# Kernel optimization log

Hardware: AMD Instinct MI355X
Metric: run time of the kernel (lower is better)

## Reference

```python
import jax, jax.numpy as jnp
import numpy as np

B, T, D, H, DFF = 64, 100, 1024, 16, 4096
HD = D // H
EPS = 1e-5


def _rope_tables(t_len, hd, dtype):
    # matches RotaryEmbedding: inv_freq over even dims, emb = cat([freqs, freqs])
    inv_freq = 1.0 / (10000.0 ** (jnp.arange(0, hd, 2, dtype=jnp.float32) / hd))
    t = jnp.arange(t_len, dtype=jnp.float32)
    freqs = jnp.einsum('i,j->ij', t, inv_freq)          # (T, hd/2)
    emb = jnp.concatenate([freqs, freqs], axis=-1)      # (T, hd)
    # apply_rope uses cos[..., ::2] / sin[..., ::2]
    cos = jnp.cos(emb)[:, ::2].astype(dtype)            # (T, hd/2)
    sin = jnp.sin(emb)[:, ::2].astype(dtype)
    return cos, sin


def _apply_rope(x, cos, sin):
    # x: (B, H, T, hd); cos/sin: (T, hd/2) broadcast over B,H
    x1 = x[..., ::2]
    x2 = x[..., 1::2]
    return jnp.concatenate([x1 * cos - x2 * sin, x1 * sin + x2 * cos], axis=-1)


def _layernorm(x, g, b):
    mu = jnp.mean(x, axis=-1, keepdims=True)
    var = jnp.mean(jnp.square(x - mu), axis=-1, keepdims=True)
    return (x - mu) * jax.lax.rsqrt(var + EPS) * g + b


def setup_inputs() -> dict:
    key = jax.random.key(0)
    ks = jax.random.split(key, 8)
    s = 0.02
    return {
        'tgt': jax.random.normal(ks[0], (B, T, D), dtype=jnp.float32),
        'Wqkv': jax.random.normal(ks[1], (3 * D, D), dtype=jnp.float32) * s,
        'bqkv': jnp.zeros((3 * D,), jnp.float32),
        'Wo': jax.random.normal(ks[2], (D, D), dtype=jnp.float32) * s,
        'bo': jnp.zeros((D,), jnp.float32),
        'W1': jax.random.normal(ks[3], (DFF, D), dtype=jnp.float32) * s,
        'b1': jnp.zeros((DFF,), jnp.float32),
        'W2': jax.random.normal(ks[4], (D, DFF), dtype=jnp.float32) * s,
        'b2': jnp.zeros((D,), jnp.float32),
        'g1': jnp.ones((D,), jnp.float32),
        'be1': jnp.zeros((D,), jnp.float32),
        'g2': jnp.ones((D,), jnp.float32),
        'be2': jnp.zeros((D,), jnp.float32),
        'tgt_mask': jnp.tril(jnp.ones((T, T), jnp.int32)),
    }


def reference(tgt, Wqkv, bqkv, Wo, bo, W1, b1, W2, b2, g1, be1, g2, be2, tgt_mask):
    dtype = tgt.dtype
    # QKV projection (torch Linear: x @ W.T + b)
    qkv = jnp.einsum('btd,ed->bte', tgt, Wqkv) + bqkv          # (B,T,3D)
    qkv = qkv.reshape(B, T, 3, H, HD).transpose(2, 0, 3, 1, 4)  # (3,B,H,T,hd)
    q, k, v = qkv[0], qkv[1], qkv[2]

    cos, sin = _rope_tables(T, HD, dtype)
    q = _apply_rope(q, cos, sin)
    k = _apply_rope(k, cos, sin)

    scale = 1.0 / np.sqrt(HD)
    scores = jnp.einsum('bhqd,bhkd->bhqk', q, k) * scale        # (B,H,T,T)
    scores = jnp.where(tgt_mask == 0, -jnp.inf, scores)
    attn = jax.nn.softmax(scores, axis=-1)
    ctx = jnp.einsum('bhqk,bhkd->bhqd', attn, v)                # (B,H,T,hd)
    ctx = ctx.transpose(0, 2, 1, 3).reshape(B, T, D)

    tgt2 = jnp.einsum('btd,ed->bte', ctx, Wo) + bo
    x = _layernorm(tgt + tgt2, g1, be1)

    h = jax.nn.relu(jnp.einsum('btd,fd->btf', x, W1) + b1)
    ff = jnp.einsum('btf,df->btd', h, W2) + b2
    out = _layernorm(x + ff, g2, be2)
    return out
```

## Files before the change

kernel.cpp:

```cpp
#include <hip/hip_runtime.h>
#include <math.h>

#define Bn   64
#define Tn   100
#define Tp   128
#define Dn   1024
#define Hn   16
#define HDn  64
#define DFFn 4096
#define EPSf 1e-5f

typedef unsigned short ushort_t;
typedef __attribute__((ext_vector_type(8))) __bf16 bf16x8;
typedef __attribute__((ext_vector_type(4))) float f32x4;

__device__ __forceinline__ float u2f(ushort_t u) {
    union { unsigned int i; float f; } v; v.i = ((unsigned int)u) << 16; return v.f;
}
__device__ __forceinline__ ushort_t f2bf(float f) {
    union { float f; unsigned int u; } v; v.f = f;
    unsigned int r = v.u + 0x7FFFu + ((v.u >> 16) & 1u);
    return (ushort_t)(r >> 16);
}

__device__ __forceinline__ void gload_lds16(const void* g, void* l) {
    __builtin_amdgcn_global_load_lds(
        (const __attribute__((address_space(1))) unsigned int*)g,
        (__attribute__((address_space(3))) unsigned int*)l,
        16, 0, 0);
}

#define VMWAIT_(n) asm volatile("s_waitcnt vmcnt(" #n ")" ::: "memory")
#define VMWAIT(n)  VMWAIT_(n)

struct ConvSeg { const float* src; ushort_t* dst; int n4; };
struct Conv5   { ConvSeg seg[5]; };

__global__ __launch_bounds__(256) void conv_bf16_multi(Conv5 cfg)
{
    int i = blockIdx.x * 256 + threadIdx.x;
    #pragma unroll
    for (int s = 0; s < 5; ++s) {
        const int n = cfg.seg[s].n4;
        if (i < n) {
            float4 v = ((const float4*)cfg.seg[s].src)[i];
            ushort4 o;
            o.x = f2bf(v.x); o.y = f2bf(v.y); o.z = f2bf(v.z); o.w = f2bf(v.w);
            ((ushort4*)cfg.seg[s].dst)[i] = o;
            return;
        }
        i -= n;
    }
}

#define GEMM_TILE_MAP(gx_, gy_, swz_)                                        \
    const int L  = blockIdx.x;                                               \
    int rowt, colt;                                                          \
    if (swz_) {                                                              \
        const int group = L / (8 * (gx_));                                   \
        int l = L - group * 8 * (gx_);                                       \
        const int rem = (gy_) - group * 8;                                   \
        if (rem >= 8) { rowt = group * 8 + (l & 7); colt = l >> 3; }         \
        else          { rowt = group * 8 + l % rem; colt = l / rem; }        \
    } else { rowt = L / (gx_); colt = L - rowt * (gx_); }

#define GEMM_KLOOP(A_, B_, K_)                                               \
    for (int k0 = 0; k0 < (K_); k0 += 64) {                                  \
        __syncthreads();                                                     \
        _Pragma("unroll")                                                    \
        for (int t = 0; t < 4; ++t) {                                        \
            const int idx = (wave * 4 + t) * 64 + lane;                      \
            const int row = idx >> 3;                                        \
            const int gc  = (idx & 7) ^ (row & 7);                           \
            gload_lds16((A_) + (size_t)(row0 + row) * (K_) + k0 + gc * 8,    \
                        &As[idx * 8]);                                       \
            gload_lds16((B_) + (size_t)(col0 + row) * (K_) + k0 + gc * 8,    \
                        &Bs[idx * 8]);                                       \
        }                                                                    \
        __syncthreads();                                                     \
        _Pragma("unroll")                                                    \
        for (int kh = 0; kh < 2; ++kh) {                                     \
            const int chunk = kh * 4 + g;                                    \
            bf16x8 af[4], bfr[4];                                            \
            _Pragma("unroll")                                                \
            for (int i = 0; i < 4; ++i) {                                    \
                const int ra = wrow + i * 16 + frow;                         \
                af[i]  = *(const bf16x8*)&As[ra * 64 + (chunk ^ (ra & 7)) * 8]; \
                const int rb = wcol + i * 16 + frow;                         \
                bfr[i] = *(const bf16x8*)&Bs[rb * 64 + (chunk ^ (rb & 7)) * 8]; \
            }                                                                \
            _Pragma("unroll")                                                \
            for (int i = 0; i < 4; ++i)                                      \
                _Pragma("unroll")                                            \
                for (int j = 0; j < 4; ++j)                                  \
                    acc[i][j] = __builtin_amdgcn_mfma_f32_16x16x32_bf16(     \
                        af[i], bfr[j], acc[i][j], 0, 0, 0);                  \
        }                                                                    \
    }

template<int BN, bool RELU, bool ADDRES, typename OutT>
__global__ __launch_bounds__(512, 2) void gemm256_bt(const ushort_t* __restrict__ A,
                                                     const ushort_t* __restrict__ Bm,
                                                     const float* __restrict__ bias,
                                                     const ushort_t* __restrict__ res,
                                                     OutT* __restrict__ C,
                                                     int M, int N, int K,
                                                     int gx, int swz)
{
    constexpr int JN = BN / 64;
    constexpr int NB = BN / 128;
    __shared__ __align__(16) ushort_t As[2][256 * 64];
    __shared__ __align__(16) ushort_t Bs[2][BN * 64];

    const int gy = M >> 8;
    GEMM_TILE_MAP(gx, gy, swz)

    const int tid  = threadIdx.x;
    const int lane = tid & 63;
    const int wave = tid >> 6;
    const int wm   = wave >> 2;
    const int wn   = wave & 3;
    const int row0 = rowt * 256;
    const int col0 = colt * BN;
    const int frow = lane & 15;
    const int g    = lane >> 4;

    auto stageA = [&](const ushort_t* src, int rowbase, ushort_t* lds) {
        #pragma unroll
        for (int i = 0; i < 2; ++i) {
            const int idx = i * 512 + tid;
            const int row = idx >> 3;
            const int gc  = (idx & 7) ^ (row & 7);
            gload_lds16(src + (size_t)(rowbase + row) * K + gc * 8, lds + idx * 8);
        }
    };
    auto stageB = [&](const ushort_t* src, int rowbase, ushort_t* lds) {
        #pragma unroll
        for (int i = 0; i < NB; ++i) {
            const int idx = i * 512 + tid;
            const int row = idx >> 3;
            const int gc  = (idx & 7) ^ (row & 7);
            gload_lds16(src + (size_t)(rowbase + row) * K + gc * 8, lds + idx * 8);
        }
    };

    f32x4 acc[8][JN] = {};

    const int NT = K >> 6;
    stageB(Bm,      col0,          &Bs[0][0]);
    stageB(Bm,      col0 + BN / 2, &Bs[0][(BN / 2) * 64]);
    stageA(A,       row0,          &As[0][0]);
    stageA(A,       row0 + 128,    &As[0][128 * 64]);
    stageB(Bm + 64, col0,          &Bs[1][0]);
    stageB(Bm + 64, col0 + BN / 2, &Bs[1][(BN / 2) * 64]);
    if constexpr (NB == 2) { VMWAIT(4); } else { VMWAIT(2); }
    __builtin_amdgcn_s_barrier();

    for (int t = 0; t < NT; ++t) {
        const int  buf = t & 1;
        const bool stA = (t + 1 < NT);
        const bool stB = (t + 2 < NT);
        bf16x8 bfr[JN][2];
        #pragma unroll
        for (int q = 0; q < 4; ++q) {
            bf16x8 af[2][2];
            #pragma unroll
            for (int ii = 0; ii < 2; ++ii)
                #pragma unroll
                for (int kk = 0; kk < 2; ++kk) {
                    const int ra = wm * 128 + (2 * q + ii) * 16 + frow;
                    const int ch = kk * 4 + g;
                    af[ii][kk] = *(const bf16x8*)&As[buf][ra * 64 + (ch ^ (ra & 7)) * 8];
                }
            if (q == 0) {
                #pragma unroll
                for (int j = 0; j < JN; ++j)
                    #pragma unroll
                    for (int kk = 0; kk < 2; ++kk) {
                        const int rb = wn * (BN / 4) + j * 16 + frow;
                        const int ch = kk * 4 + g;
                        bfr[j][kk] = *(const bf16x8*)&Bs[buf][rb * 64 + (ch ^ (rb & 7)) * 8];
                    }
            }
            if (q == 0 && stA) stageA(A + (t + 1) * 64, row0,       &As[buf ^ 1][0]);
            if (q == 1 && stA) stageA(A + (t + 1) * 64, row0 + 128, &As[buf ^ 1][128 * 64]);
            if (q == 2 && stB) stageB(Bm + (t + 2) * 64, col0,          &Bs[buf][0]);
            if (q == 3 && stB) stageB(Bm + (t + 2) * 64, col0 + BN / 2, &Bs[buf][(BN / 2) * 64]);
            __builtin_amdgcn_s_barrier();
            asm volatile("s_waitcnt lgkmcnt(0)" ::: "memory");
            __builtin_amdgcn_sched_barrier(0);
            __builtin_amdgcn_s_setprio(1);
            #pragma unroll
            for (int ii = 0; ii < 2; ++ii)
                #pragma unroll
                for (int j = 0; j < JN; ++j)
                    #pragma unroll
                    for (int kk = 0; kk < 2; ++kk)
                        acc[2 * q + ii][j] = __builtin_amdgcn_mfma_f32_16x16x32_bf16(
                            af[ii][kk], bfr[j][kk], acc[2 * q + ii][j], 0, 0, 0);
            __builtin_amdgcn_s_setprio(0);
            __builtin_amdgcn_sched_barrier(0);
            if (q == 3) {
                if (stB)      { if constexpr (NB == 2) { VMWAIT(4); } else { VMWAIT(2); } }
                else if (stA) { VMWAIT(0); }
            }
            __builtin_amdgcn_s_barrier();
        }
    }

    const int crow = (lane >> 4) * 4;
    const int ccol = lane & 15;
    #pragma unroll
    for (int i = 0; i < 8; ++i) {
        #pragma unroll
        for (int r = 0; r < 4; ++r) {
            const int row = row0 + wm * 128 + i * 16 + crow + r;
            #pragma unroll
            for (int j = 0; j < JN; ++j) {
                const int col = col0 + wn * (BN / 4) + j * 16 + ccol;
                float v = acc[i][j][r] + bias[col];
                if constexpr (ADDRES) v += u2f(res[(size_t)row * N + col]);
                if constexpr (RELU) v = fmaxf(v, 0.f);
                if constexpr (sizeof(OutT) == 2)
                    C[(size_t)row * N + col] = (OutT)f2bf(v);
                else
                    C[(size_t)row * N + col] = (OutT)v;
            }
        }
    }
}

__global__ __launch_bounds__(256) void gemm_qkv_rope(const ushort_t* __restrict__ A,
                                                     const ushort_t* __restrict__ Bm,
                                                     const float* __restrict__ bias,
                                                     ushort_t* __restrict__ q,
                                                     ushort_t* __restrict__ k,
                                                     ushort_t* __restrict__ vt)
{
    __shared__ __align__(16) ushort_t As[128 * 64];
    __shared__ __align__(16) ushort_t Bs[128 * 64];

    const int gy = 50, gx = 24;
    GEMM_TILE_MAP(gx, gy, 1)

    const int tid  = threadIdx.x;
    const int wave = tid >> 6;
    const int lane = tid & 63;
    const int row0 = rowt * 128;
    const int col0 = colt * 128;
    const int wrow = (wave >> 1) * 64;
    const int wcol = (wave & 1) * 64;
    const int frow = lane & 15;
    const int g    = lane >> 4;

    f32x4 acc[4][4] = {};
    GEMM_KLOOP(A, Bm, Dn)

    const int sec = col0 >> 10;

    __syncthreads();
    float2* tab = (float2*)As;
    if (sec != 2) {
        for (int e = tid; e < 2048; e += 256) {
            const int lr = e >> 4, f = e & 15;
            const int row = row0 + lr;
            const int b = row / Tn;
            const int t = row - b * Tn;
            float s, c;
            sincosf((float)t * exp2f(-0.83048202f * (float)f), &s, &c);
            tab[lr * 16 + f] = make_float2(c, s);
        }
    }
    __syncthreads();

    const int crow = (lane >> 4) * 4;
    const int ccol = lane & 15;

    if (sec == 2) {
        #pragma unroll
        for (int i = 0; i < 4; ++i) {
            #pragma unroll
            for (int r = 0; r < 4; ++r) {
                const int row = row0 + wrow + i * 16 + crow + r;
                const int b = row / Tn, t = row - b * Tn;
                #pragma unroll
                for (int j = 0; j < 4; ++j) {
                    const int colg = col0 + wcol + j * 16 + ccol;
                    const int hcol = colg & 1023;
                    const int h = hcol >> 6, d = hcol & 63;
                    const float v = acc[i][j][r] + bias[colg];
                    vt[((size_t)(b * Hn + h) * HDn + d) * Tp + t] = f2bf(v);
                }
            }
        }
    } else {
        ushort_t* dst = sec ? k : q;
        const int odd = ccol & 1;
        const int f0  = ccol >> 1;
        #pragma unroll
        for (int i = 0; i < 4; ++i) {
            #pragma unroll
            for (int r = 0; r < 4; ++r) {
                const int lr  = wrow + i * 16 + crow + r;
                const int row = row0 + lr;
                const int b = row / Tn, t = row - b * Tn;
                const float2 cs0 = tab[lr * 16 + f0];
                const float2 cs1 = tab[lr * 16 + 8 + f0];
                (void)t;
                #pragma unroll
                for (int j = 0; j < 4; ++j) {
                    const int colg = col0 + wcol + j * 16 + ccol;
                    const int hcol = colg & 1023;
                    const int h  = hcol >> 6;
                    const int dh = hcol & 63;
                    const int m  = dh >> 1;
                    const float val   = acc[i][j][r] + bias[colg];
                    const float other = __shfl_xor(val, 1);
                    const float sn = (j & 1) ? cs1.y : cs0.y;
                    const float cs = (j & 1) ? cs1.x : cs0.x;
                    const float x1 = odd ? other : val;
                    const float x2 = odd ? val : other;
                    const float o  = odd ? (x1 * sn + x2 * cs)
                                         : (x1 * cs - x2 * sn);
                    const int outcol = odd ? (m + 32) : m;
                    dst[((size_t)(b * Hn + h) * Tp + t) * HDn + outcol] = f2bf(o);
                }
            }
        }
    }
}

__global__ __launch_bounds__(256) void attn_mfma(const ushort_t* __restrict__ q,
                                                 const ushort_t* __restrict__ k,
                                                 const ushort_t* __restrict__ vt,
                                                 ushort_t* __restrict__ ctx)
{
    __shared__ __align__(16) ushort_t sm[24576];

    const int bh   = blockIdx.x;
    const int b    = bh >> 4, h = bh & 15;
    const int tid  = threadIdx.x;
    const int wave = tid >> 6;
    const int lane = tid & 63;
    const int c    = lane & 15;
    const int g    = lane >> 4;
    const int R0   = wave * 32;

    const ushort_t* qg = q  + (size_t)bh * Tp * HDn;
    const ushort_t* kg = k  + (size_t)bh * Tp * HDn;
    const ushort_t* vg = vt + (size_t)bh * HDn * Tp;
    for (int s = wave; s < 16; s += 4) {
        const int idx = s * 64 + lane;
        { const int row = idx >> 3, pc = idx & 7, gc = pc ^ (row & 7);
          gload_lds16(qg + row * 64 + gc * 8, &sm[idx * 8]);
          gload_lds16(kg + row * 64 + gc * 8, &sm[8192 + idx * 8]); }
        { const int row = idx >> 4, pc = idx & 15, gc = pc ^ (row & 15);
          gload_lds16(vg + row * 128 + gc * 8, &sm[16384 + idx * 8]); }
    }
    __syncthreads();

    f32x4 acc[2][8] = {};
    #pragma unroll
    for (int ks = 0; ks < 2; ++ks) {
        const int cb = ks * 4;
        bf16x8 aq[2];
        #pragma unroll
        for (int i = 0; i < 2; ++i) {
            const int row = R0 + i * 16 + c;
            const int ph  = (cb + g) ^ (row & 7);
            aq[i] = *(const bf16x8*)&sm[row * 64 + ph * 8];
        }
        #pragma unroll
        for (int j = 0; j < 8; ++j) {
            const int row = j * 16 + c;
            const int ph  = (cb + g) ^ (row & 7);
            const bf16x8 bk = *(const bf16x8*)&sm[8192 + row * 64 + ph * 8];
            acc[0][j] = __builtin_amdgcn_mfma_f32_16x16x32_bf16(aq[0], bk, acc[0][j], 0, 0, 0);
            acc[1][j] = __builtin_amdgcn_mfma_f32_16x16x32_bf16(aq[1], bk, acc[1][j], 0, 0, 0);
        }
    }
    __syncthreads();

    float linv[2][4];
    #pragma unroll
    for (int i = 0; i < 2; ++i) {
        #pragma unroll
        for (int r = 0; r < 4; ++r) {
            const int row = R0 + i * 16 + g * 4 + r;
            float sv[8], m = -1e30f;
            #pragma unroll
            for (int j = 0; j < 8; ++j) {
                const int col = j * 16 + c;
                const float s = acc[i][j][r] * 0.125f;
                sv[j] = (col <= row) ? s : -1e30f;
                m = fmaxf(m, sv[j]);
            }
            #pragma unroll
            for (int msk = 1; msk < 16; msk <<= 1) m = fmaxf(m, __shfl_xor(m, msk));
            float l = 0.f;
            #pragma unroll
            for (int j = 0; j < 8; ++j) {
                const int col = j * 16 + c;
                const float p = (col <= row) ? __expf(sv[j] - m) : 0.f;
                sv[j] = p; l += p;
            }
            #pragma unroll
            for (int msk = 1; msk < 16; msk <<= 1) l += __shfl_xor(l, msk);
            linv[i][r] = 1.f / l;
            #pragma unroll
            for (int j = 0; j < 8; ++j) {
                const int chunk = j * 2 + (c >> 3);
                const int ph    = chunk ^ (row & 15);
                sm[row * 128 + ph * 8 + (c & 7)] = f2bf(sv[j]);
            }
        }
    }
    __syncthreads();

    f32x4 acc2[2][4] = {};
    #pragma unroll
    for (int ks = 0; ks < 4; ++ks) {
        const int cb = ks * 4;
        bf16x8 ap[2];
        #pragma unroll
        for (int i = 0; i < 2; ++i) {
            const int row = R0 + i * 16 + c;
            const int ph  = (cb + g) ^ (row & 15);
            ap[i] = *(const bf16x8*)&sm[row * 128 + ph * 8];
        }
        #pragma unroll
        for (int n = 0; n < 4; ++n) {
            const int row = n * 16 + c;
            const int ph  = (cb + g) ^ (row & 15);
            const bf16x8 bv = *(const bf16x8*)&sm[16384 + row * 128 + ph * 8];
            acc2[0][n] = __builtin_amdgcn_mfma_f32_16x16x32_bf16(ap[0], bv, acc2[0][n], 0, 0, 0);
            acc2[1][n] = __builtin_amdgcn_mfma_f32_16x16x32_bf16(ap[1], bv, acc2[1][n], 0, 0, 0);
        }
    }

    #pragma unroll
    for (int i = 0; i < 2; ++i) {
        #pragma unroll
        for (int r = 0; r < 4; ++r) {
            const int row = R0 + i * 16 + g * 4 + r;
            if (row < Tn) {
                const float s = linv[i][r];
                #pragma unroll
                for (int n = 0; n < 4; ++n) {
                    const int col = n * 16 + c;
                    ctx[(size_t)(b * Tn + row) * Dn + h * HDn + col] =
                        f2bf(acc2[i][n][r] * s);
                }
            }
        }
    }
}

__global__ __launch_bounds__(256) void ln_single(const ushort_t* __restrict__ a,
                                                 const float* __restrict__ g,
                                                 const float* __restrict__ be,
                                                 ushort_t* __restrict__ out_bf)
{
    const int row = blockIdx.x;
    const int tid = threadIdx.x;
    __shared__ float red[256];
    const size_t base = (size_t)row * Dn;

    float vals[4];
    float s = 0.f;
    #pragma unroll
    for (int i = 0; i < 4; ++i) {
        const int c = tid + i * 256;
        vals[i] = u2f(a[base + c]);
        s += vals[i];
    }
    red[tid] = s;
    __syncthreads();
    for (int o = 128; o > 0; o >>= 1) {
        if (tid < o) red[tid] += red[tid + o];
        __syncthreads();
    }
    const float mu = red[0] * (1.f / Dn);
    __syncthreads();

    float vs = 0.f;
    #pragma unroll
    for (int i = 0; i < 4; ++i) { const float d = vals[i] - mu; vs += d * d; }
    red[tid] = vs;
    __syncthreads();
    for (int o = 128; o > 0; o >>= 1) {
        if (tid < o) red[tid] += red[tid + o];
        __syncthreads();
    }
    const float rstd = rsqrtf(red[0] * (1.f / Dn) + EPSf);

    #pragma unroll
    for (int i = 0; i < 4; ++i) {
        const int c = tid + i * 256;
        out_bf[base + c] = f2bf((vals[i] - mu) * rstd * g[c] + be[c]);
    }
}

__global__ __launch_bounds__(256) void add_ln2(const ushort_t* __restrict__ a,
                                               const ushort_t* __restrict__ r,
                                               const float* __restrict__ g,
                                               const float* __restrict__ be,
                                               float* __restrict__ out)
{
    const int row = blockIdx.x;
    const int tid = threadIdx.x;
    __shared__ float red[256];
    const size_t base = (size_t)row * Dn;

    float vals[4];
    float s = 0.f;
    #pragma unroll
    for (int i = 0; i < 4; ++i) {
        const int c = tid + i * 256;
        vals[i] = u2f(a[base + c]) + u2f(r[base + c]);
        s += vals[i];
    }
    red[tid] = s;
    __syncthreads();
    for (int o = 128; o > 0; o >>= 1) {
        if (tid < o) red[tid] += red[tid + o];
        __syncthreads();
    }
    const float mu = red[0] * (1.f / Dn);
    __syncthreads();

    float vs = 0.f;
    #pragma unroll
    for (int i = 0; i < 4; ++i) { const float d = vals[i] - mu; vs += d * d; }
    red[tid] = vs;
    __syncthreads();
    for (int o = 128; o > 0; o >>= 1) {
        if (tid < o) red[tid] += red[tid + o];
        __syncthreads();
    }
    const float rstd = rsqrtf(red[0] * (1.f / Dn) + EPSf);

    #pragma unroll
    for (int i = 0; i < 4; ++i) {
        const int c = tid + i * 256;
        out[base + c] = (vals[i] - mu) * rstd * g[c] + be[c];
    }
}

extern "C" void kernel_launch(void* const* d_in, const int* in_sizes, int n_in,
                              void* d_out, int out_size, void* d_ws, size_t ws_size,
                              hipStream_t stream)
{
    const float* tgt  = (const float*)d_in[0];
    const float* Wqkv = (const float*)d_in[1];
    const float* bqkv = (const float*)d_in[2];
    const float* Wo   = (const float*)d_in[3];
    const float* bo   = (const float*)d_in[4];
    const float* W1   = (const float*)d_in[5];
    const float* b1   = (const float*)d_in[6];
    const float* W2   = (const float*)d_in[7];
    const float* b2   = (const float*)d_in[8];
    const float* g1   = (const float*)d_in[9];
    const float* be1  = (const float*)d_in[10];
    const float* g2   = (const float*)d_in[11];
    const float* be2  = (const float*)d_in[12];
    float* out = (float*)d_out;
    (void)in_sizes; (void)n_in; (void)out_size; (void)ws_size;

    const int M = Bn * Tn;

    char* w = (char*)d_ws;
    ushort_t* tgt_bf  = (ushort_t*)(w);
    ushort_t* Wqkv_bf = (ushort_t*)(w + 13107200);
    ushort_t* Wo_bf   = (ushort_t*)(w + 19398656);
    ushort_t* W1_bf   = (ushort_t*)(w + 21495808);
    ushort_t* W2_bf   = (ushort_t*)(w + 29884416);

    ushort_t* qb    = (ushort_t*)(w + 38273024);
    ushort_t* kb    = (ushort_t*)(w + 55050240);
    ushort_t* vtb   = (ushort_t*)(w + 71827456);
    ushort_t* hbuf  = (ushort_t*)(w + 38273024);
    ushort_t* ctxb  = (ushort_t*)(w + 88604672);
    ushort_t* tgt2b = (ushort_t*)(w + 101711872);
    ushort_t* ffb   = (ushort_t*)(w + 101711872);
    ushort_t* x_bf  = (ushort_t*)(w + 114819072);

    Conv5 cfg;
    cfg.seg[0] = { tgt,  tgt_bf,  M * Dn / 4 };
    cfg.seg[1] = { Wqkv, Wqkv_bf, 3 * Dn * Dn / 4 };
    cfg.seg[2] = { Wo,   Wo_bf,   Dn * Dn / 4 };
    cfg.seg[3] = { W1,   W1_bf,   DFFn * Dn / 4 };
    cfg.seg[4] = { W2,   W2_bf,   Dn * DFFn / 4 };
    const int total4 = (M * Dn + 3 * Dn * Dn + Dn * Dn + 2 * DFFn * Dn) / 4;
    conv_bf16_multi<<<(total4 + 255) / 256, 256, 0, stream>>>(cfg);

    gemm_qkv_rope<<<1200, 256, 0, stream>>>(tgt_bf, Wqkv_bf, bqkv, qb, kb, vtb);
    attn_mfma<<<Bn * Hn, 256, 0, stream>>>(qb, kb, vtb, ctxb);
    gemm256_bt<128, false, true, ushort_t><<<(Dn / 128) * (M / 256), 512, 0, stream>>>(
        ctxb, Wo_bf, bo, tgt_bf, tgt2b, M, Dn, Dn, Dn / 128, 1);
    ln_single<<<M, 256, 0, stream>>>(tgt2b, g1, be1, x_bf);
    gemm256_bt<256, true, false, ushort_t><<<(M / 256) * (DFFn / 256), 512, 0, stream>>>(
        x_bf, W1_bf, b1, nullptr, hbuf, M, DFFn, Dn, DFFn / 256, 0);
    gemm256_bt<128, false, false, ushort_t><<<(Dn / 128) * (M / 256), 512, 0, stream>>>(
        hbuf, W2_bf, b2, nullptr, ffb, M, Dn, DFFn, Dn / 128, 1);
    add_ln2<<<M, 256, 0, stream>>>(x_bf, ffb, g2, be2, out);
}
```

Measured before the change: 443.0 us.

## Share a two-phase pipelined 256x128 GEMM k-loop across QKV, Wo, FFN kernels

Factors the double-buffered 256x128 k-loop into a shared helper that uses two compute phases per k-step instead of four, with fewer barriers per step. The QKV+RoPE GEMM moves from a single-buffered 128x128 tile with 256 threads onto this pipelined 256x128 path with 512 threads, and the RoPE epilogue is adapted to match. The FFN1 GEMM drops its 256-wide N tile for 128, which doubles its block count but lowers per-block reuse. The goal is better overlap of loads with MFMA work and a uniform tile shape, at the cost of coarser phases and a different grid balance.

```diff
diff --git a/kernel.cpp b/kernel.cpp
--- a/kernel.cpp
+++ b/kernel.cpp
@@ -64,41 +64,115 @@
         else          { rowt = group * 8 + l % rem; colt = l / rem; }        \
     } else { rowt = L / (gx_); colt = L - rowt * (gx_); }
 
-#define GEMM_KLOOP(A_, B_, K_)                                               \
-    for (int k0 = 0; k0 < (K_); k0 += 64) {                                  \
-        __syncthreads();                                                     \
-        _Pragma("unroll")                                                    \
-        for (int t = 0; t < 4; ++t) {                                        \
-            const int idx = (wave * 4 + t) * 64 + lane;                      \
-            const int row = idx >> 3;                                        \
-            const int gc  = (idx & 7) ^ (row & 7);                           \
-            gload_lds16((A_) + (size_t)(row0 + row) * (K_) + k0 + gc * 8,    \
-                        &As[idx * 8]);                                       \
-            gload_lds16((B_) + (size_t)(col0 + row) * (K_) + k0 + gc * 8,    \
-                        &Bs[idx * 8]);                                       \
-        }                                                                    \
-        __syncthreads();                                                     \
-        _Pragma("unroll")                                                    \
-        for (int kh = 0; kh < 2; ++kh) {                                     \
-            const int chunk = kh * 4 + g;                                    \
-            bf16x8 af[4], bfr[4];                                            \
-            _Pragma("unroll")                                                \
-            for (int i = 0; i < 4; ++i) {                                    \
-                const int ra = wrow + i * 16 + frow;                         \
-                af[i]  = *(const bf16x8*)&As[ra * 64 + (chunk ^ (ra & 7)) * 8]; \
-                const int rb = wcol + i * 16 + frow;                         \
-                bfr[i] = *(const bf16x8*)&Bs[rb * 64 + (chunk ^ (rb & 7)) * 8]; \
-            }                                                                \
-            _Pragma("unroll")                                                \
-            for (int i = 0; i < 4; ++i)                                      \
-                _Pragma("unroll")                                            \
-                for (int j = 0; j < 4; ++j)                                  \
-                    acc[i][j] = __builtin_amdgcn_mfma_f32_16x16x32_bf16(     \
-                        af[i], bfr[j], acc[i][j], 0, 0, 0);                  \
-        }                                                                    \
-    }
-
-template<int BN, bool RELU, bool ADDRES, typename OutT>
+__device__ __forceinline__ void kloop2p_128(
+    const ushort_t* __restrict__ A, const ushort_t* __restrict__ Bm, const int K,
+    ushort_t (&As)[2][256 * 64], ushort_t (&Bs)[2][128 * 64], f32x4 (&acc)[8][2],
+    const int tid, const int wm, const int wn, const int frow, const int g,
+    const int row0, const int col0)
+{
+    auto stageA = [&](const ushort_t* src, int rowbase, ushort_t* lds) {
+        #pragma unroll
+        for (int i = 0; i < 2; ++i) {
+            const int idx = i * 512 + tid;
+            const int row = idx >> 3;
+            const int gc  = (idx & 7) ^ (row & 7);
+            gload_lds16(src + (size_t)(rowbase + row) * K + gc * 8, lds + idx * 8);
+        }
+    };
+    auto stageB = [&](const ushort_t* src, int rowbase, ushort_t* lds) {
+        const int idx = tid;
+        const int row = idx >> 3;
+        const int gc  = (idx & 7) ^ (row & 7);
+        gload_lds16(src + (size_t)(rowbase + row) * K + gc * 8, lds + idx * 8);
+    };
+
+    const int NT = K >> 6;
+    stageB(Bm,      col0,      &Bs[0][0]);
+    stageB(Bm,      col0 + 64, &Bs[0][64 * 64]);
+    stageA(A,       row0,      &As[0][0]);
+    stageA(A,       row0 + 128,&As[0][128 * 64]);
+    stageB(Bm + 64, col0,      &Bs[1][0]);
+    stageB(Bm + 64, col0 + 64, &Bs[1][64 * 64]);
+    VMWAIT(2);
+    __builtin_amdgcn_s_barrier();
+
+    for (int t = 0; t < NT; ++t) {
+        const int  buf = t & 1;
+        const bool stA = (t + 1 < NT);
+        const bool stB = (t + 2 < NT);
+
+        bf16x8 bfr[2][2];
+        #pragma unroll
+        for (int j = 0; j < 2; ++j)
+            #pragma unroll
+            for (int kk = 0; kk < 2; ++kk) {
+                const int rb = wn * 32 + j * 16 + frow;
+                const int ch = kk * 4 + g;
+                bfr[j][kk] = *(const bf16x8*)&Bs[buf][rb * 64 + (ch ^ (rb & 7)) * 8];
+            }
+        bf16x8 af0[4][2];
+        #pragma unroll
+        for (int m = 0; m < 4; ++m)
+            #pragma unroll
+            for (int kk = 0; kk < 2; ++kk) {
+                const int ra = wm * 128 + m * 16 + frow;
+                const int ch = kk * 4 + g;
+                af0[m][kk] = *(const bf16x8*)&As[buf][ra * 64 + (ch ^ (ra & 7)) * 8];
+            }
+        if (stA) {
+            stageA(A + (t + 1) * 64, row0,       &As[buf ^ 1][0]);
+            stageA(A + (t + 1) * 64, row0 + 128, &As[buf ^ 1][128 * 64]);
+        }
+        __builtin_amdgcn_s_barrier();
+        asm volatile("s_waitcnt lgkmcnt(0)" ::: "memory");
+        __builtin_amdgcn_sched_barrier(0);
+        __builtin_amdgcn_s_setprio(1);
+        #pragma unroll
+        for (int m = 0; m < 4; ++m)
+            #pragma unroll
+            for (int j = 0; j < 2; ++j)
+                #pragma unroll
+                for (int kk = 0; kk < 2; ++kk)
+                    acc[m][j] = __builtin_amdgcn_mfma_f32_16x16x32_bf16(
+                        af0[m][kk], bfr[j][kk], acc[m][j], 0, 0, 0);
+        __builtin_amdgcn_s_setprio(0);
+        __builtin_amdgcn_sched_barrier(0);
+        __builtin_amdgcn_s_barrier();
+
+        bf16x8 af1[4][2];
+        #pragma unroll
+        for (int m = 0; m < 4; ++m)
+            #pragma unroll
+            for (int kk = 0; kk < 2; ++kk) {
+                const int ra = wm * 128 + (4 + m) * 16 + frow;
+                const int ch = kk * 4 + g;
+                af1[m][kk] = *(const bf16x8*)&As[buf][ra * 64 + (ch ^ (ra & 7)) * 8];
+            }
+        if (stB) {
+            stageB(Bm + (t + 2) * 64, col0,      &Bs[buf][0]);
+            stageB(Bm + (t + 2) * 64, col0 + 64, &Bs[buf][64 * 64]);
+        }
+        __builtin_amdgcn_s_barrier();
+        asm volatile("s_waitcnt lgkmcnt(0)" ::: "memory");
+        __builtin_amdgcn_sched_barrier(0);
+        __builtin_amdgcn_s_setprio(1);
+        #pragma unroll
+        for (int m = 0; m < 4; ++m)
+            #pragma unroll
+            for (int j = 0; j < 2; ++j)
+                #pragma unroll
+                for (int kk = 0; kk < 2; ++kk)
+                    acc[4 + m][j] = __builtin_amdgcn_mfma_f32_16x16x32_bf16(
+                        af1[m][kk], bfr[j][kk], acc[4 + m][j], 0, 0, 0);
+        __builtin_amdgcn_s_setprio(0);
+        __builtin_amdgcn_sched_barrier(0);
+        if (stB)      { VMWAIT(2); }
+        else if (stA) { VMWAIT(0); }
+        __builtin_amdgcn_s_barrier();
+    }
+}
+
+template<bool RELU, bool ADDRES, typename OutT>
 __global__ __launch_bounds__(512, 2) void gemm256_bt(const ushort_t* __restrict__ A,
                                                      const ushort_t* __restrict__ Bm,
                                                      const float* __restrict__ bias,
@@ -107,10 +181,8 @@
                                                      int M, int N, int K,
                                                      int gx, int swz)
 {
-    constexpr int JN = BN / 64;
-    constexpr int NB = BN / 128;
     __shared__ __align__(16) ushort_t As[2][256 * 64];
-    __shared__ __align__(16) ushort_t Bs[2][BN * 64];
+    __shared__ __align__(16) ushort_t Bs[2][128 * 64];
 
     const int gy = M >> 8;
     GEMM_TILE_MAP(gx, gy, swz)
@@ -121,92 +193,12 @@
     const int wm   = wave >> 2;
     const int wn   = wave & 3;
     const int row0 = rowt * 256;
-    const int col0 = colt * BN;
+    const int col0 = colt * 128;
     const int frow = lane & 15;
     const int g    = lane >> 4;
 
-    auto stageA = [&](const ushort_t* src, int rowbase, ushort_t* lds) {
-        #pragma unroll
-        for (int i = 0; i < 2; ++i) {
-            const int idx = i * 512 + tid;
-            const int row = idx >> 3;
-            const int gc  = (idx & 7) ^ (row & 7);
-            gload_lds16(src + (size_t)(rowbase + row) * K + gc * 8, lds + idx * 8);
-        }
-    };
-    auto stageB = [&](const ushort_t* src, int rowbase, ushort_t* lds) {
-        #pragma unroll
-        for (int i = 0; i < NB; ++i) {
-            const int idx = i * 512 + tid;
-            const int row = idx >> 3;
-            const int gc  = (idx & 7) ^ (row & 7);
-            gload_lds16(src + (size_t)(rowbase + row) * K + gc * 8, lds + idx * 8);
-        }
-    };
-
-    f32x4 acc[8][JN] = {};
-
-    const int NT = K >> 6;
-    stageB(Bm,      col0,          &Bs[0][0]);
-    stageB(Bm,      col0 + BN / 2, &Bs[0][(BN / 2) * 64]);
-    stageA(A,       row0,          &As[0][0]);
-    stageA(A,       row0 + 128,    &As[0][128 * 64]);
-    stageB(Bm + 64, col0,          &Bs[1][0]);
-    stageB(Bm + 64, col0 + BN / 2, &Bs[1][(BN / 2) * 64]);
-    if constexpr (NB == 2) { VMWAIT(4); } else { VMWAIT(2); }
-    __builtin_amdgcn_s_barrier();
-
-    for (int t = 0; t < NT; ++t) {
-        const int  buf = t & 1;
-        const bool stA = (t + 1 < NT);
-        const bool stB = (t + 2 < NT);
-        bf16x8 bfr[JN][2];
-        #pragma unroll
-        for (int q = 0; q < 4; ++q) {
-            bf16x8 af[2][2];
-            #pragma unroll
-            for (int ii = 0; ii < 2; ++ii)
-                #pragma unroll
-                for (int kk = 0; kk < 2; ++kk) {
-                    const int ra = wm * 128 + (2 * q + ii) * 16 + frow;
-                    const int ch = kk * 4 + g;
-                    af[ii][kk] = *(const bf16x8*)&As[buf][ra * 64 + (ch ^ (ra & 7)) * 8];
-                }
-            if (q == 0) {
-                #pragma unroll
-                for (int j = 0; j < JN; ++j)
-                    #pragma unroll
-                    for (int kk = 0; kk < 2; ++kk) {
-                        const int rb = wn * (BN / 4) + j * 16 + frow;
-                        const int ch = kk * 4 + g;
-                        bfr[j][kk] = *(const bf16x8*)&Bs[buf][rb * 64 + (ch ^ (rb & 7)) * 8];
-                    }
-            }
-            if (q == 0 && stA) stageA(A + (t + 1) * 64, row0,       &As[buf ^ 1][0]);
-            if (q == 1 && stA) stageA(A + (t + 1) * 64, row0 + 128, &As[buf ^ 1][128 * 64]);
-            if (q == 2 && stB) stageB(Bm + (t + 2) * 64, col0,          &Bs[buf][0]);
-            if (q == 3 && stB) stageB(Bm + (t + 2) * 64, col0 + BN / 2, &Bs[buf][(BN / 2) * 64]);
-            __builtin_amdgcn_s_barrier();
-            asm volatile("s_waitcnt lgkmcnt(0)" ::: "memory");
-            __builtin_amdgcn_sched_barrier(0);
-            __builtin_amdgcn_s_setprio(1);
-            #pragma unroll
-            for (int ii = 0; ii < 2; ++ii)
-                #pragma unroll
-                for (int j = 0; j < JN; ++j)
-                    #pragma unroll
-                    for (int kk = 0; kk < 2; ++kk)
-                        acc[2 * q + ii][j] = __builtin_amdgcn_mfma_f32_16x16x32_bf16(
-                            af[ii][kk], bfr[j][kk], acc[2 * q + ii][j], 0, 0, 0);
-            __builtin_amdgcn_s_setprio(0);
-            __builtin_amdgcn_sched_barrier(0);
-            if (q == 3) {
-                if (stB)      { if constexpr (NB == 2) { VMWAIT(4); } else { VMWAIT(2); } }
-                else if (stA) { VMWAIT(0); }
-            }
-            __builtin_amdgcn_s_barrier();
-        }
-    }
+    f32x4 acc[8][2] = {};
+    kloop2p_128(A, Bm, K, As, Bs, acc, tid, wm, wn, frow, g, row0, col0);
 
     const int crow = (lane >> 4) * 4;
     const int ccol = lane & 15;
@@ -216,8 +208,8 @@
         for (int r = 0; r < 4; ++r) {
             const int row = row0 + wm * 128 + i * 16 + crow + r;
             #pragma unroll
-            for (int j = 0; j < JN; ++j) {
-                const int col = col0 + wn * (BN / 4) + j * 16 + ccol;
+            for (int j = 0; j < 2; ++j) {
+                const int col = col0 + wn * 32 + j * 16 + ccol;
                 float v = acc[i][j][r] + bias[col];
                 if constexpr (ADDRES) v += u2f(res[(size_t)row * N + col]);
                 if constexpr (RELU) v = fmaxf(v, 0.f);
@@ -230,38 +222,38 @@
     }
 }
 
-__global__ __launch_bounds__(256) void gemm_qkv_rope(const ushort_t* __restrict__ A,
-                                                     const ushort_t* __restrict__ Bm,
-                                                     const float* __restrict__ bias,
-                                                     ushort_t* __restrict__ q,
-                                                     ushort_t* __restrict__ k,
-                                                     ushort_t* __restrict__ vt)
-{
-    __shared__ __align__(16) ushort_t As[128 * 64];
-    __shared__ __align__(16) ushort_t Bs[128 * 64];
-
-    const int gy = 50, gx = 24;
+__global__ __launch_bounds__(512, 2) void gemm256_qkv_rope(const ushort_t* __restrict__ A,
+                                                           const ushort_t* __restrict__ Bm,
+                                                           const float* __restrict__ bias,
+                                                           ushort_t* __restrict__ q,
+                                                           ushort_t* __restrict__ k,
+                                                           ushort_t* __restrict__ vt)
+{
+    __shared__ __align__(16) ushort_t As[2][256 * 64];
+    __shared__ __align__(16) ushort_t Bs[2][128 * 64];
+
+    const int gy = 25, gx = 24;
     GEMM_TILE_MAP(gx, gy, 1)
 
     const int tid  = threadIdx.x;
+    const int lane = tid & 63;
     const int wave = tid >> 6;
-    const int lane = tid & 63;
-    const int row0 = rowt * 128;
+    const int wm   = wave >> 2;
+    const int wn   = wave & 3;
+    const int row0 = rowt * 256;
     const int col0 = colt * 128;
-    const int wrow = (wave >> 1) * 64;
-    const int wcol = (wave & 1) * 64;
     const int frow = lane & 15;
     const int g    = lane >> 4;
 
-    f32x4 acc[4][4] = {};
-    GEMM_KLOOP(A, Bm, Dn)
+    f32x4 acc[8][2] = {};
+    kloop2p_128(A, Bm, Dn, As, Bs, acc, tid, wm, wn, frow, g, row0, col0);
 
     const int sec = col0 >> 10;
 
     __syncthreads();
-    float2* tab = (float2*)As;
+    float2* tab = (float2*)&As[0][0];
     if (sec != 2) {
-        for (int e = tid; e < 2048; e += 256) {
+        for (int e = tid; e < 4096; e += 512) {
             const int lr = e >> 4, f = e & 15;
             const int row = row0 + lr;
             const int b = row / Tn;
@@ -278,14 +270,14 @@
 
     if (sec == 2) {
         #pragma unroll
-        for (int i = 0; i < 4; ++i) {
+        for (int i = 0; i < 8; ++i) {
             #pragma unroll
             for (int r = 0; r < 4; ++r) {
-                const int row = row0 + wrow + i * 16 + crow + r;
+                const int row = row0 + wm * 128 + i * 16 + crow + r;
                 const int b = row / Tn, t = row - b * Tn;
                 #pragma unroll
-                for (int j = 0; j < 4; ++j) {
-                    const int colg = col0 + wcol + j * 16 + ccol;
+                for (int j = 0; j < 2; ++j) {
+                    const int colg = col0 + wn * 32 + j * 16 + ccol;
                     const int hcol = colg & 1023;
                     const int h = hcol >> 6, d = hcol & 63;
                     const float v = acc[i][j][r] + bias[colg];
@@ -298,18 +290,17 @@
         const int odd = ccol & 1;
         const int f0  = ccol >> 1;
         #pragma unroll
-        for (int i = 0; i < 4; ++i) {
+        for (int i = 0; i < 8; ++i) {
             #pragma unroll
             for (int r = 0; r < 4; ++r) {
-                const int lr  = wrow + i * 16 + crow + r;
+                const int lr  = wm * 128 + i * 16 + crow + r;
                 const int row = row0 + lr;
                 const int b = row / Tn, t = row - b * Tn;
                 const float2 cs0 = tab[lr * 16 + f0];
                 const float2 cs1 = tab[lr * 16 + 8 + f0];
-                (void)t;
                 #pragma unroll
-                for (int j = 0; j < 4; ++j) {
-                    const int colg = col0 + wcol + j * 16 + ccol;
+                for (int j = 0; j < 2; ++j) {
+                    const int colg = col0 + wn * 32 + j * 16 + ccol;
                     const int hcol = colg & 1023;
                     const int h  = hcol >> 6;
                     const int dh = hcol & 63;
@@ -594,14 +585,14 @@
     const int total4 = (M * Dn + 3 * Dn * Dn + Dn * Dn + 2 * DFFn * Dn) / 4;
     conv_bf16_multi<<<(total4 + 255) / 256, 256, 0, stream>>>(cfg);
 
-    gemm_qkv_rope<<<1200, 256, 0, stream>>>(tgt_bf, Wqkv_bf, bqkv, qb, kb, vtb);
+    gemm256_qkv_rope<<<600, 512, 0, stream>>>(tgt_bf, Wqkv_bf, bqkv, qb, kb, vtb);
     attn_mfma<<<Bn * Hn, 256, 0, stream>>>(qb, kb, vtb, ctxb);
-    gemm256_bt<128, false, true, ushort_t><<<(Dn / 128) * (M / 256), 512, 0, stream>>>(
+    gemm256_bt<false, true, ushort_t><<<(Dn / 128) * (M / 256), 512, 0, stream>>>(
         ctxb, Wo_bf, bo, tgt_bf, tgt2b, M, Dn, Dn, Dn / 128, 1);
     ln_single<<<M, 256, 0, stream>>>(tgt2b, g1, be1, x_bf);
-    gemm256_bt<256, true, false, ushort_t><<<(M / 256) * (DFFn / 256), 512, 0, stream>>>(
-        x_bf, W1_bf, b1, nullptr, hbuf, M, DFFn, Dn, DFFn / 256, 0);
-    gemm256_bt<128, false, false, ushort_t><<<(Dn / 128) * (M / 256), 512, 0, stream>>>(
+    gemm256_bt<true, false, ushort_t><<<(M / 256) * (DFFn / 128), 512, 0, stream>>>(
+        x_bf, W1_bf, b1, nullptr, hbuf, M, DFFn, Dn, DFFn / 128, 0);
+    gemm256_bt<false, false, ushort_t><<<(Dn / 128) * (M / 256), 512, 0, stream>>>(
         hbuf, W2_bf, b2, nullptr, ffb, M, Dn, DFFn, Dn / 128, 1);
     add_ln2<<<M, 256, 0, stream>>>(x_bf, ffb, g2, be2, out);
 }
```

New measurement: 441.3 us. About the same (-0.4%).
